# Kernel tuning notes

Measured on AMD Instinct MI355X. Metric: run time of the kernel, lower is better.

## Reference

```python
import jax, jax.numpy as jnp
import numpy as np

N = 1048576          # total octree nodes across the batch
C = 64               # in_channels
BATCH_SIZE = 16
GROUP = 16           # clamped: min_group_channels(4)*group(32) > 64 -> group = 64//4
CPG = C // GROUP     # channels_per_group = 4
EPS = 1e-5


def setup_inputs() -> dict:
    key = jax.random.key(0)
    k1, k2, k3, k4 = jax.random.split(key, 4)
    data = jax.random.normal(k1, (N, C), dtype=jnp.float32)
    batch_id = jnp.sort(jax.random.randint(k2, (N,), 0, BATCH_SIZE)).astype(jnp.int32)
    weights = jax.random.normal(k3, (1, C), dtype=jnp.float32)
    bias = jax.random.normal(k4, (1, C), dtype=jnp.float32)
    return {"data": data, "batch_id": batch_id, "weights": weights, "bias": bias}


def _adjust_for_group(t):
    # sum over channels within each group, broadcast back to all channels
    if CPG > 1:
        t = t.reshape(-1, GROUP, CPG).sum(-1, keepdims=True)
        t = jnp.broadcast_to(t, (t.shape[0], GROUP, CPG)).reshape(-1, C)
    return t


def reference(data, batch_id, weights, bias):
    # per-sample element counts, scaled so the group-sum of means is a true group mean
    ones = jnp.ones((data.shape[0],), dtype=data.dtype)
    count = jax.ops.segment_sum(ones, batch_id, num_segments=BATCH_SIZE)[:, None]  # [B,1]
    count = count * CPG
    inv_count = 1.0 / (count + EPS)

    mean = jax.ops.segment_sum(data, batch_id, num_segments=BATCH_SIZE) * inv_count  # [B,C]
    mean = _adjust_for_group(mean)
    out = data - mean[batch_id]  # gather broadcast [N,C]

    var = jax.ops.segment_sum(out * out, batch_id, num_segments=BATCH_SIZE) * inv_count
    var = _adjust_for_group(var)
    inv_std = jax.lax.rsqrt(var + EPS)

    out = out * inv_std[batch_id]
    return out * weights + bias
```

## Files before the change

kernel.cpp:

```cpp
#include <hip/hip_runtime.h>

#define NBATCH 16
#define NCH 64
#define CPG 4
#define NGRP 16
#define EPSV 1e-5f


__global__ void ogn_stats(const float* __restrict__ data,
                          const int* __restrict__ bid,
                          float* __restrict__ S1,
                          float* __restrict__ S2,
                          int* __restrict__ cnt,
                          int N, int rows_per_block) {
    __shared__ float ls1[NBATCH * NCH];
    __shared__ float ls2[NBATCH * NCH];
    __shared__ int   lcnt[NBATCH];

    for (int i = threadIdx.x; i < NBATCH * NCH; i += blockDim.x) {
        ls1[i] = 0.f;
        ls2[i] = 0.f;
    }
    if (threadIdx.x < NBATCH) lcnt[threadIdx.x] = 0;
    __syncthreads();

    const int t     = threadIdx.x;
    const int c4    = t & 15;
    const int rlane = t >> 4;

    long long row_begin = (long long)blockIdx.x * rows_per_block;
    long long row_end   = row_begin + rows_per_block;
    if (row_end > N) row_end = N;

    const float4* data4 = (const float4*)data;

    float4 s1 = make_float4(0.f, 0.f, 0.f, 0.f);
    float4 s2 = make_float4(0.f, 0.f, 0.f, 0.f);
    int cur = -1;
    int c   = 0;

    for (long long r = row_begin + rlane; r < row_end; r += 16) {
        int b = bid[r];
        if (b != cur) {
            if (cur >= 0) {
                int base = cur * NCH + c4 * 4;
                atomicAdd(&ls1[base + 0], s1.x);
                atomicAdd(&ls1[base + 1], s1.y);
                atomicAdd(&ls1[base + 2], s1.z);
                atomicAdd(&ls1[base + 3], s1.w);
                atomicAdd(&ls2[base + 0], s2.x);
                atomicAdd(&ls2[base + 1], s2.y);
                atomicAdd(&ls2[base + 2], s2.z);
                atomicAdd(&ls2[base + 3], s2.w);
                if (c4 == 0) atomicAdd(&lcnt[cur], c);
            }
            s1 = make_float4(0.f, 0.f, 0.f, 0.f);
            s2 = make_float4(0.f, 0.f, 0.f, 0.f);
            c = 0;
            cur = b;
        }
        float4 v = data4[r * 16 + c4];
        s1.x += v.x; s1.y += v.y; s1.z += v.z; s1.w += v.w;
        s2.x += v.x * v.x; s2.y += v.y * v.y; s2.z += v.z * v.z; s2.w += v.w * v.w;
        c++;
    }
    if (cur >= 0) {
        int base = cur * NCH + c4 * 4;
        atomicAdd(&ls1[base + 0], s1.x);
        atomicAdd(&ls1[base + 1], s1.y);
        atomicAdd(&ls1[base + 2], s1.z);
        atomicAdd(&ls1[base + 3], s1.w);
        atomicAdd(&ls2[base + 0], s2.x);
        atomicAdd(&ls2[base + 1], s2.y);
        atomicAdd(&ls2[base + 2], s2.z);
        atomicAdd(&ls2[base + 3], s2.w);
        if (c4 == 0) atomicAdd(&lcnt[cur], c);
    }
    __syncthreads();

    for (int i = threadIdx.x; i < NBATCH * NCH; i += blockDim.x) {
        float v1 = ls1[i];
        float v2 = ls2[i];
        if (v1 != 0.f) atomicAdd(&S1[i], v1);
        if (v2 != 0.f) atomicAdd(&S2[i], v2);
    }
    if (threadIdx.x < NBATCH) {
        int v = lcnt[threadIdx.x];
        if (v != 0) atomicAdd(&cnt[threadIdx.x], v);
    }
}

__global__ void ogn_params(const float* __restrict__ S1,
                           const float* __restrict__ S2,
                           const int* __restrict__ cnt,
                           const float* __restrict__ w,
                           const float* __restrict__ bias,
                           float* __restrict__ A,
                           float* __restrict__ B) {
    int t = threadIdx.x;
    if (t >= NBATCH * NGRP) return;
    int b = t >> 4;
    int g = t & 15;

    int base = b * NCH + g * CPG;
    float s1g = 0.f, s2g = 0.f;
#pragma unroll
    for (int k = 0; k < CPG; ++k) {
        s1g += S1[base + k];
        s2g += S2[base + k];
    }
    float countf    = (float)cnt[b] * (float)CPG;
    float inv_count = 1.f / (countf + EPSV);
    float mean      = s1g * inv_count;
    float var       = inv_count * (s2g - 2.f * mean * s1g + countf * mean * mean);
    float inv_std   = rsqrtf(var + EPSV);

#pragma unroll
    for (int k = 0; k < CPG; ++k) {
        int ch = g * CPG + k;
        float wv = w[ch];
        float bv = bias[ch];
        A[b * NCH + ch] = inv_std * wv;
        B[b * NCH + ch] = bv - mean * inv_std * wv;
    }
}

__global__ void ogn_apply(const float* __restrict__ data,
                          const int* __restrict__ bid,
                          const float* __restrict__ A,
                          const float* __restrict__ B,
                          float* __restrict__ out,
                          long long total4) {
    const float4* d4 = (const float4*)data;
    const float4* A4 = (const float4*)A;
    const float4* B4 = (const float4*)B;
    float4* o4 = (float4*)out;

    long long i      = (long long)blockIdx.x * blockDim.x + threadIdx.x;
    long long stride = (long long)gridDim.x * blockDim.x;

    for (; i < total4; i += stride) {
        long long row = i >> 4;
        int c4 = (int)(i & 15);
        int b  = bid[row];
        float4 v  = d4[i];
        float4 a  = A4[b * 16 + c4];
        float4 bb = B4[b * 16 + c4];
        float4 r;
        r.x = fmaf(v.x, a.x, bb.x);
        r.y = fmaf(v.y, a.y, bb.y);
        r.z = fmaf(v.z, a.z, bb.z);
        r.w = fmaf(v.w, a.w, bb.w);
        o4[i] = r;
    }
}

extern "C" void kernel_launch(void* const* d_in, const int* in_sizes, int n_in,
                              void* d_out, int out_size, void* d_ws, size_t ws_size,
                              hipStream_t stream) {
    const float* data = (const float*)d_in[0];
    const int*   bid  = (const int*)d_in[1];
    const float* w    = (const float*)d_in[2];
    const float* bias = (const float*)d_in[3];
    float* out = (float*)d_out;

    int N = in_sizes[1];

    char* ws = (char*)d_ws;
    float* S1  = (float*)(ws + 0);
    float* S2  = (float*)(ws + 4096);
    int*   cnt = (int*)  (ws + 8192);
    float* A   = (float*)(ws + 8448);
    float* B   = (float*)(ws + 12544);

    hipMemsetAsync(d_ws, 0, 8256, stream);

    const int NB1 = 1024;
    int rows_per_block = (N + NB1 - 1) / NB1;
    ogn_stats<<<NB1, 256, 0, stream>>>(data, bid, S1, S2, cnt, N, rows_per_block);

    ogn_params<<<1, 256, 0, stream>>>(S1, S2, cnt, w, bias, A, B);

    long long total4 = (long long)N * (NCH / 4);
    int NB3 = 8192;
    ogn_apply<<<NB3, 256, 0, stream>>>(data, bid, A, B, out, total4);
}
```

Before: 514.9 us.

## Fuse stats, params and apply into one cooperative kernel with grid syncs

Replaces the memset and the three separate kernels with a single cooperative kernel. Each block zeroes the global accumulators, syncs the grid, reduces its rows, syncs again, then computes the per-batch scale and shift into shared memory and applies them to its own row range. This removes the launch and memset overheads, and the second pass over each block's slice may hit in cache. The cost is two grid-wide barriers, and the cooperative launch requires all 1024 blocks to be co-resident.

```diff
diff --git a/kernel.cpp b/kernel.cpp
--- a/kernel.cpp
+++ b/kernel.cpp
@@ -1,30 +1,43 @@
 #include <hip/hip_runtime.h>
+#include <hip/hip_cooperative_groups.h>
+
+namespace cg = cooperative_groups;
 
 #define NBATCH 16
 #define NCH 64
-#define CPG 4
 #define NGRP 16
+#define CPGV 4
 #define EPSV 1e-5f
+#define GRID_BLKS 1024
 
 
-__global__ void ogn_stats(const float* __restrict__ data,
-                          const int* __restrict__ bid,
-                          float* __restrict__ S1,
-                          float* __restrict__ S2,
-                          int* __restrict__ cnt,
-                          int N, int rows_per_block) {
-    __shared__ float ls1[NBATCH * NCH];
-    __shared__ float ls2[NBATCH * NCH];
-    __shared__ int   lcnt[NBATCH];
+__global__ void __launch_bounds__(256, 4)
+ogn_fused(const float* __restrict__ data,
+          const int* __restrict__ bidp,
+          const float* __restrict__ w,
+          const float* __restrict__ bias,
+          float* __restrict__ out,
+          float* __restrict__ S1,
+          float* __restrict__ S2,
+          int* __restrict__ cnt,
+          int N, int rows_per_block) {
+    cg::grid_group grid = cg::this_grid();
 
-    for (int i = threadIdx.x; i < NBATCH * NCH; i += blockDim.x) {
-        ls1[i] = 0.f;
-        ls2[i] = 0.f;
-    }
-    if (threadIdx.x < NBATCH) lcnt[threadIdx.x] = 0;
-    __syncthreads();
+    __shared__ __align__(16) float ls1[NBATCH * NCH];
+    __shared__ __align__(16) float ls2[NBATCH * NCH];
+    __shared__ int lcnt[NBATCH];
 
-    const int t     = threadIdx.x;
+    const int t = threadIdx.x;
+
+    long long gtid = (long long)blockIdx.x * blockDim.x + t;
+    if (gtid < NBATCH * NCH) { S1[gtid] = 0.f; S2[gtid] = 0.f; }
+    if (gtid < NBATCH) cnt[gtid] = 0;
+
+    for (int i = t; i < NBATCH * NCH; i += 256) { ls1[i] = 0.f; ls2[i] = 0.f; }
+    if (t < NBATCH) lcnt[t] = 0;
+
+    grid.sync();
+
     const int c4    = t & 15;
     const int rlane = t >> 4;
 
@@ -40,7 +53,7 @@
     int c   = 0;
 
     for (long long r = row_begin + rlane; r < row_end; r += 16) {
-        int b = bid[r];
+        int b = bidp[r];
         if (b != cur) {
             if (cur >= 0) {
                 int base = cur * NCH + c4 * 4;
@@ -78,80 +91,64 @@
     }
     __syncthreads();
 
-    for (int i = threadIdx.x; i < NBATCH * NCH; i += blockDim.x) {
+    for (int i = t; i < NBATCH * NCH; i += 256) {
         float v1 = ls1[i];
         float v2 = ls2[i];
         if (v1 != 0.f) atomicAdd(&S1[i], v1);
         if (v2 != 0.f) atomicAdd(&S2[i], v2);
     }
-    if (threadIdx.x < NBATCH) {
-        int v = lcnt[threadIdx.x];
-        if (v != 0) atomicAdd(&cnt[threadIdx.x], v);
+    if (t < NBATCH) {
+        int v = lcnt[t];
+        if (v != 0) atomicAdd(&cnt[t], v);
     }
-}
 
-__global__ void ogn_params(const float* __restrict__ S1,
-                           const float* __restrict__ S2,
-                           const int* __restrict__ cnt,
-                           const float* __restrict__ w,
-                           const float* __restrict__ bias,
-                           float* __restrict__ A,
-                           float* __restrict__ B) {
-    int t = threadIdx.x;
-    if (t >= NBATCH * NGRP) return;
-    int b = t >> 4;
-    int g = t & 15;
+    grid.sync();
 
-    int base = b * NCH + g * CPG;
-    float s1g = 0.f, s2g = 0.f;
+    {
+        int b = t >> 4;
+        int g = t & 15;
+        int base = b * NCH + g * CPGV;
+        float s1g = 0.f, s2g = 0.f;
 #pragma unroll
-    for (int k = 0; k < CPG; ++k) {
-        s1g += S1[base + k];
-        s2g += S2[base + k];
+        for (int k = 0; k < CPGV; ++k) {
+            s1g += S1[base + k];
+            s2g += S2[base + k];
+        }
+        float countf    = (float)cnt[b] * (float)CPGV;
+        float inv_count = 1.f / (countf + EPSV);
+        float mean      = s1g * inv_count;
+        float var       = inv_count * (s2g - 2.f * mean * s1g + countf * mean * mean);
+        float inv_std   = rsqrtf(var + EPSV);
+#pragma unroll
+        for (int k = 0; k < CPGV; ++k) {
+            int ch = g * CPGV + k;
+            float a = inv_std * w[ch];
+            ls1[b * NCH + ch] = a;
+            ls2[b * NCH + ch] = bias[ch] - mean * a;
+        }
     }
-    float countf    = (float)cnt[b] * (float)CPG;
-    float inv_count = 1.f / (countf + EPSV);
-    float mean      = s1g * inv_count;
-    float var       = inv_count * (s2g - 2.f * mean * s1g + countf * mean * mean);
-    float inv_std   = rsqrtf(var + EPSV);
+    __syncthreads();
 
-#pragma unroll
-    for (int k = 0; k < CPG; ++k) {
-        int ch = g * CPG + k;
-        float wv = w[ch];
-        float bv = bias[ch];
-        A[b * NCH + ch] = inv_std * wv;
-        B[b * NCH + ch] = bv - mean * inv_std * wv;
-    }
-}
+    float4* out4 = (float4*)out;
+    cur = -1;
+    float4 av = make_float4(0.f, 0.f, 0.f, 0.f);
+    float4 bv = make_float4(0.f, 0.f, 0.f, 0.f);
 
-__global__ void ogn_apply(const float* __restrict__ data,
-                          const int* __restrict__ bid,
-                          const float* __restrict__ A,
-                          const float* __restrict__ B,
-                          float* __restrict__ out,
-                          long long total4) {
-    const float4* d4 = (const float4*)data;
-    const float4* A4 = (const float4*)A;
-    const float4* B4 = (const float4*)B;
-    float4* o4 = (float4*)out;
-
-    long long i      = (long long)blockIdx.x * blockDim.x + threadIdx.x;
-    long long stride = (long long)gridDim.x * blockDim.x;
-
-    for (; i < total4; i += stride) {
-        long long row = i >> 4;
-        int c4 = (int)(i & 15);
-        int b  = bid[row];
-        float4 v  = d4[i];
-        float4 a  = A4[b * 16 + c4];
-        float4 bb = B4[b * 16 + c4];
-        float4 r;
-        r.x = fmaf(v.x, a.x, bb.x);
-        r.y = fmaf(v.y, a.y, bb.y);
-        r.z = fmaf(v.z, a.z, bb.z);
-        r.w = fmaf(v.w, a.w, bb.w);
-        o4[i] = r;
+    for (long long r = row_begin + rlane; r < row_end; r += 16) {
+        int b = bidp[r];
+        if (b != cur) {
+            cur = b;
+            int base = b * NCH + c4 * 4;
+            av = *(const float4*)&ls1[base];
+            bv = *(const float4*)&ls2[base];
+        }
+        float4 v = data4[r * 16 + c4];
+        float4 o;
+        o.x = fmaf(v.x, av.x, bv.x);
+        o.y = fmaf(v.y, av.y, bv.y);
+        o.z = fmaf(v.z, av.z, bv.z);
+        o.w = fmaf(v.w, av.w, bv.w);
+        out4[r * 16 + c4] = o;
     }
 }
 
@@ -170,18 +167,12 @@
     float* S1  = (float*)(ws + 0);
     float* S2  = (float*)(ws + 4096);
     int*   cnt = (int*)  (ws + 8192);
-    float* A   = (float*)(ws + 8448);
-    float* B   = (float*)(ws + 12544);
 
-    hipMemsetAsync(d_ws, 0, 8256, stream);
+    int rows_per_block = (N + GRID_BLKS - 1) / GRID_BLKS;
 
-    const int NB1 = 1024;
-    int rows_per_block = (N + NB1 - 1) / NB1;
-    ogn_stats<<<NB1, 256, 0, stream>>>(data, bid, S1, S2, cnt, N, rows_per_block);
-
-    ogn_params<<<1, 256, 0, stream>>>(S1, S2, cnt, w, bias, A, B);
-
-    long long total4 = (long long)N * (NCH / 4);
-    int NB3 = 8192;
-    ogn_apply<<<NB3, 256, 0, stream>>>(data, bid, A, B, out, total4);
+    void* args[] = { (void*)&data, (void*)&bid, (void*)&w, (void*)&bias,
+                     (void*)&out, (void*)&S1, (void*)&S2, (void*)&cnt,
+                     (void*)&N, (void*)&rows_per_block };
+    hipLaunchCooperativeKernel((void*)ogn_fused, dim3(GRID_BLKS), dim3(256),
+                               args, 0, stream);
 }
```

Result: slower. 674.1 us (+30.9%).
